# Performance work log

Measured on AMD Instinct MI355X. Metric: run time of the kernel, lower is better.

Reference implementation:

```python
import jax, jax.numpy as jnp
import numpy as np

INPUT_SIZE = 968
HIDDEN = 128
ESP = 1e-6


def _gru_scan(xp, w_hh, b_hh):
    # xp: [T, B, 3H] precomputed input projections; returns [T, B, H]
    B = xp.shape[1]
    h0 = jnp.zeros((B, HIDDEN), dtype=xp.dtype)

    def step(h, xp_t):
        gi_r, gi_z, gi_n = jnp.split(xp_t, 3, axis=-1)
        gh = h @ w_hh.T + b_hh
        gh_r, gh_z, gh_n = jnp.split(gh, 3, axis=-1)
        r = jax.nn.sigmoid(gi_r + gh_r)
        z = jax.nn.sigmoid(gi_z + gh_z)
        n = jnp.tanh(gi_n + r * gh_n)
        h_new = (1.0 - z) * n + z * h
        return h_new, h_new

    _, hs = jax.lax.scan(step, h0, xp)
    return hs


def _bigru_ln(x, w_ih_f, w_hh_f, b_ih_f, b_hh_f,
              w_ih_b, w_hh_b, b_ih_b, b_hh_b, ln_w, ln_b):
    # x: [B, T, D] (batch_first)
    # precompute input projections as one big GEMM per direction
    xp_f = jnp.einsum('btd,gd->btg', x, w_ih_f) + b_ih_f  # [B,T,3H]
    xp_b = jnp.einsum('btd,gd->btg', x, w_ih_b) + b_ih_b
    xp_f = jnp.swapaxes(xp_f, 0, 1)  # [T,B,3H]
    xp_b = jnp.swapaxes(xp_b, 0, 1)[::-1]  # reversed time for backward dir

    h_f = _gru_scan(xp_f, w_hh_f, b_hh_f)          # [T,B,H]
    h_b = _gru_scan(xp_b, w_hh_b, b_hh_b)[::-1]    # [T,B,H], un-reverse

    out = jnp.concatenate([h_f, h_b], axis=-1)     # [T,B,2H]
    out = jnp.swapaxes(out, 0, 1)                  # [B,T,2H]

    # LayerNormal: uses unbiased std (torch.std default, ddof=1), clamped
    mu = jnp.mean(out, axis=-1, keepdims=True)
    sigma = jnp.std(out, axis=-1, keepdims=True, ddof=1)
    sigma = jnp.maximum(sigma, ESP)
    return (out - mu) / sigma * ln_w + ln_b


def setup_inputs() -> dict:
    key = jax.random.key(0)
    ks = jax.random.split(key, 10)
    B, T = 64, 512
    s_ih = 1.0 / np.sqrt(HIDDEN)
    u = lambda k, shape: jax.random.uniform(k, shape, jnp.float32, -s_ih, s_ih)
    return {
        'x': jax.random.normal(ks[0], (B, T, INPUT_SIZE), jnp.float32),
        'w_ih_f': u(ks[1], (3 * HIDDEN, INPUT_SIZE)),
        'w_hh_f': u(ks[2], (3 * HIDDEN, HIDDEN)),
        'b_ih_f': u(ks[3], (3 * HIDDEN,)),
        'b_hh_f': u(ks[4], (3 * HIDDEN,)),
        'w_ih_b': u(ks[5], (3 * HIDDEN, INPUT_SIZE)),
        'w_hh_b': u(ks[6], (3 * HIDDEN, HIDDEN)),
        'b_ih_b': u(ks[7], (3 * HIDDEN,)),
        'b_hh_b': u(ks[8], (3 * HIDDEN,)),
        'ln_w': jnp.ones((2 * HIDDEN,), jnp.float32),
        'ln_b': jnp.zeros((2 * HIDDEN,), jnp.float32),
    }


def reference(x, w_ih_f, w_hh_f, b_ih_f, b_hh_f,
              w_ih_b, w_hh_b, b_ih_b, b_hh_b, ln_w, ln_b):
    return _bigru_ln(x, w_ih_f, w_hh_f, b_ih_f, b_hh_f,
                     w_ih_b, w_hh_b, b_ih_b, b_hh_b, ln_w, ln_b)
```

## Files before the change

kernel.cpp:

```cpp
#include <hip/hip_runtime.h>
#include <stdint.h>


#define LOG2E 1.4426950408889634f
#define TT 512
#define D_IN 968
#define KP 992
#define NOUT 768
#define HID 128

typedef __attribute__((ext_vector_type(8))) short short8;
typedef __attribute__((ext_vector_type(4))) float f32x4;
typedef __attribute__((ext_vector_type(4))) unsigned int u32x4;
typedef __attribute__((ext_vector_type(2))) unsigned int u32x2;

__device__ __forceinline__ unsigned short f2bf(float f) {
  unsigned u = __builtin_bit_cast(unsigned, f);
  u += 0x7FFFu + ((u >> 16) & 1u);
  return (unsigned short)(u >> 16);
}
__device__ __forceinline__ unsigned pack2bf(float a, float b) {
  return (unsigned)f2bf(a) | ((unsigned)f2bf(b) << 16);
}
__device__ __forceinline__ float exp2_(float x) { return __builtin_amdgcn_exp2f(x); }
__device__ __forceinline__ float rcp_(float x)  { return __builtin_amdgcn_rcpf(x); }

__device__ __forceinline__ void async_load16(const void* g, void* l) {
  __builtin_amdgcn_global_load_lds(
      (const __attribute__((address_space(1))) unsigned int*)g,
      (__attribute__((address_space(3))) unsigned int*)l, 16, 0, 0);
}

__device__ __forceinline__ void wg_barrier_lds() {
  asm volatile("s_waitcnt lgkmcnt(0)\n\ts_barrier" ::: "memory");
}

#define WIH_BYTES (NOUT * KP * 2)
#define WHH_BYTES (NOUT * HID * 2)
#define BIAS_BYTES 3072
#define BASE_OFF (WIH_BYTES + WHH_BYTES + BIAS_BYTES)
#define XBF_BYTES ((size_t)32768 * KP * 2)
#define XP_BYTES ((size_t)32768 * NOUT * 4)

__global__ __launch_bounds__(256) void kx_convert(const float* __restrict__ X,
                                                  unsigned short* __restrict__ Xb) {
  const long row = blockIdx.x;
  const int t = threadIdx.x;
  if (t < 242) {
    f32x4 v = *(const f32x4*)(X + row * D_IN + t * 4);
    u32x2 p = {pack2bf(v.x, v.y), pack2bf(v.z, v.w)};
    *(u32x2*)(Xb + row * KP + t * 4) = p;
  } else if (t < 248) {
    *(u32x2*)(Xb + row * KP + t * 4) = (u32x2){0, 0};
  }
}

__global__ __launch_bounds__(256) void k0_convert(
    const float* __restrict__ wihf, const float* __restrict__ whhf,
    const float* __restrict__ bihf, const float* __restrict__ wihb,
    const float* __restrict__ whhb, const float* __restrict__ bihb,
    unsigned short* __restrict__ wih16, unsigned short* __restrict__ whh16,
    float* __restrict__ bias_s) {
  int blk = blockIdx.x, tid = threadIdx.x;
  if (blk < NOUT) {
    int n = blk;
    float sc = ((n % 384) < 256) ? LOG2E : 2.0f * LOG2E;
    const float* src = (n < 384) ? (wihf + (long)n * D_IN) : (wihb + (long)(n - 384) * D_IN);
    for (int c = 0; c < 4; c++) {
      int k = c * 256 + tid;
      if (k < KP) {
        float v = (k < D_IN) ? src[k] * sc : 0.0f;
        wih16[(long)n * KP + k] = f2bf(v);
      }
    }
  } else if (blk < NOUT + 96) {
    int e0 = ((blk - NOUT) * 256 + tid) * 4;
    for (int i = 0; i < 4; i++) {
      int e = e0 + i;
      int m = e >> 7, k = e & 127;
      float sc = ((m % 384) < 256) ? LOG2E : 2.0f * LOG2E;
      float v = (m < 384) ? whhf[m * HID + k] : whhb[(m - 384) * HID + k];
      whh16[e] = f2bf(v * sc);
    }
  } else {
    for (int c = 0; c < 3; c++) {
      int n = c * 256 + tid;
      if (n < NOUT) {
        float sc = ((n % 384) < 256) ? LOG2E : 2.0f * LOG2E;
        bias_s[n] = ((n < 384) ? bihf[n] : bihb[n - 384]) * sc;
      }
    }
  }
}

__global__ __launch_bounds__(256, 2) void k1_gemm_fast(
    const unsigned short* __restrict__ Xb, const unsigned short* __restrict__ W,
    const float* __restrict__ bias_s, float* __restrict__ XP) {
  __shared__ unsigned short As[128 * 32];
  __shared__ unsigned short Bs[128 * 32];

  const int tid = threadIdx.x;
  const int lane = tid & 63, w = tid >> 6;
  const int q = lane >> 4, l15 = lane & 15;
  const int wr = w >> 1, wc = w & 1;
  const int nt = blockIdx.x;
  const int mt = blockIdx.y;
  const long R0 = (long)mt * 128;
  const int C0 = nt * 128;

  f32x4 acc[4][4];
#pragma unroll
  for (int i = 0; i < 4; i++)
#pragma unroll
    for (int j = 0; j < 4; j++) acc[i][j] = {0.f, 0.f, 0.f, 0.f};

  for (int it = 0; it < 31; it++) {
    const int k0 = it * 32;
#pragma unroll
    for (int c = 0; c < 2; c++) {
      int idx = c * 256 + w * 64 + lane;
      int row = idx >> 2, koff = (idx & 3) * 8;
      async_load16(Xb + (R0 + row) * KP + k0 + koff,
                   ((char*)As) + (c * 256 + w * 64) * 16);
      async_load16(W + (long)(C0 + row) * KP + k0 + koff,
                   ((char*)Bs) + (c * 256 + w * 64) * 16);
    }
    __syncthreads();
    short8 af[4], bf[4];
#pragma unroll
    for (int i = 0; i < 4; i++)
      af[i] = *(const short8*)&As[(wr * 64 + i * 16 + l15) * 32 + q * 8];
#pragma unroll
    for (int j = 0; j < 4; j++)
      bf[j] = *(const short8*)&Bs[(wc * 64 + j * 16 + l15) * 32 + q * 8];
#pragma unroll
    for (int i = 0; i < 4; i++)
#pragma unroll
      for (int j = 0; j < 4; j++)
        acc[i][j] = __builtin_amdgcn_mfma_f32_16x16x32_bf16(af[i], bf[j], acc[i][j], 0, 0, 0);
    __syncthreads();
  }
  float bv[4];
#pragma unroll
  for (int j = 0; j < 4; j++) bv[j] = bias_s[C0 + wc * 64 + j * 16 + l15];
#pragma unroll
  for (int i = 0; i < 4; i++)
#pragma unroll
    for (int j = 0; j < 4; j++) {
      int col = C0 + wc * 64 + j * 16 + l15;
      long Rb = R0 + wr * 64 + i * 16 + q * 4;
#pragma unroll
      for (int r = 0; r < 4; r++)
        XP[(Rb + r) * NOUT + col] = acc[i][j][r] + bv[j];
    }
}

#define AS_STRIDE 40
__global__ __launch_bounds__(256, 2) void k1_gemm_slow(
    const float* __restrict__ X, const unsigned short* __restrict__ W,
    const float* __restrict__ bias_s, float* __restrict__ XP) {
  __shared__ unsigned short As[128 * AS_STRIDE];
  __shared__ unsigned short Bs[128 * 32];
  const int tid = threadIdx.x;
  const int lane = tid & 63, w = tid >> 6;
  const int q = lane >> 4, l15 = lane & 15;
  const int wr = w >> 1, wc = w & 1;
  const int nt = blockIdx.x, mt = blockIdx.y;
  const long R0 = (long)mt * 128;
  const int C0 = nt * 128;
  const int ar = tid >> 1, ahf = tid & 1;
  f32x4 acc[4][4];
#pragma unroll
  for (int i = 0; i < 4; i++)
#pragma unroll
    for (int j = 0; j < 4; j++) acc[i][j] = {0.f, 0.f, 0.f, 0.f};
  const float* arow = X + (R0 + ar) * D_IN;
  for (int it = 0; it < 31; it++) {
    int k0 = it * 32;
    unsigned pk[8];
#pragma unroll
    for (int c = 0; c < 4; c++) {
      int kc = k0 + ahf * 16 + c * 4;
      kc = (kc <= 964) ? kc : 964;
      f32x4 v = *(const f32x4*)(arow + kc);
      pk[c * 2 + 0] = pack2bf(v.x, v.y);
      pk[c * 2 + 1] = pack2bf(v.z, v.w);
    }
    unsigned short* adst = &As[ar * AS_STRIDE + ahf * 16];
    *(u32x4*)adst = (u32x4){pk[0], pk[1], pk[2], pk[3]};
    *(u32x4*)(adst + 8) = (u32x4){pk[4], pk[5], pk[6], pk[7]};
#pragma unroll
    for (int c = 0; c < 2; c++) {
      int idx = c * 256 + w * 64 + lane;
      int brow = idx >> 2, koff = (idx & 3) * 8;
      async_load16(W + (long)(C0 + brow) * KP + k0 + koff,
                   ((char*)Bs) + (c * 256 + w * 64) * 16);
    }
    __syncthreads();
    short8 af[4], bf[4];
#pragma unroll
    for (int i = 0; i < 4; i++)
      af[i] = *(const short8*)&As[(wr * 64 + i * 16 + l15) * AS_STRIDE + q * 8];
#pragma unroll
    for (int j = 0; j < 4; j++)
      bf[j] = *(const short8*)&Bs[(wc * 64 + j * 16 + l15) * 32 + q * 8];
#pragma unroll
    for (int i = 0; i < 4; i++)
#pragma unroll
      for (int j = 0; j < 4; j++)
        acc[i][j] = __builtin_amdgcn_mfma_f32_16x16x32_bf16(af[i], bf[j], acc[i][j], 0, 0, 0);
    __syncthreads();
  }
  float bv[4];
#pragma unroll
  for (int j = 0; j < 4; j++) bv[j] = bias_s[C0 + wc * 64 + j * 16 + l15];
#pragma unroll
  for (int i = 0; i < 4; i++)
#pragma unroll
    for (int j = 0; j < 4; j++) {
      int col = C0 + wc * 64 + j * 16 + l15;
      long Rb = R0 + wr * 64 + i * 16 + q * 4;
#pragma unroll
      for (int r = 0; r < 4; r++)
        XP[(Rb + r) * NOUT + col] = acc[i][j][r] + bv[j];
    }
}

#define GI_STRIDE 52

__global__ __launch_bounds__(512) void k2_gru(
    const unsigned short* __restrict__ WHH, const float* __restrict__ XP,
    const float* __restrict__ bhh_f, const float* __restrict__ bhh_b,
    float* __restrict__ OUT) {
  __shared__ unsigned short Hl[2][16 * 128];
  __shared__ float GIl[2][8][16 * GI_STRIDE];

  const int tid = threadIdx.x;
  const int lane = tid & 63, w = tid >> 6;
  const int q = lane >> 4, b = lane & 15;
  const int dir = blockIdx.x & 1, bg = blockIdx.x >> 1;
  const int j0 = w * 16 + q * 4;

  for (int i = tid; i < 2 * 16 * 128; i += 512) ((unsigned short*)Hl)[i] = 0;

  short8 afr[3][4];
#pragma unroll
  for (int g = 0; g < 3; g++)
#pragma unroll
    for (int kt = 0; kt < 4; kt++) {
      int row = dir * 384 + g * 128 + w * 16 + b;
      afr[g][kt] = *(const short8*)(WHH + (long)row * HID + kt * 32 + q * 8);
    }
  const float* bhh = dir ? bhh_b : bhh_f;
  f32x4 bh[3];
#pragma unroll
  for (int g = 0; g < 3; g++) {
    f32x4 t = *(const f32x4*)(bhh + g * 128 + j0);
    bh[g] = t * ((g < 2) ? LOG2E : 2.0f * LOG2E);
  }

  const int lb = lane >> 2, lc = lane & 3;
  const long gi_base = (long)(bg * 16 + lb) * TT * NOUT + dir * 384 + w * 16 + lc * 4;
  const long out_base = (long)(bg * 16 + b) * TT * 256 + dir * 128 + j0;

  f32x4 gp0, gp1, gp2;
  {
    const int td0 = dir ? (TT - 1) : 0;
    const float* gb = XP + gi_base + (long)td0 * NOUT;
    f32x4 a0 = *(const f32x4*)(gb);
    f32x4 a1 = *(const f32x4*)(gb + 128);
    f32x4 a2 = *(const f32x4*)(gb + 256);
    float* giw0 = &GIl[0][w][lb * GI_STRIDE + lc * 4];
    *(f32x4*)(giw0 + 0) = a0;
    *(f32x4*)(giw0 + 16) = a1;
    *(f32x4*)(giw0 + 32) = a2;
    const int td1 = dir ? (TT - 2) : 1;
    const float* gb1 = XP + gi_base + (long)td1 * NOUT;
    gp0 = *(const f32x4*)(gb1);
    gp1 = *(const f32x4*)(gb1 + 128);
    gp2 = *(const f32x4*)(gb1 + 256);
  }
  f32x4 h = {0.f, 0.f, 0.f, 0.f};
  __syncthreads();

  for (int t = 0; t < TT; t++) {
    const int cur = t & 1, nxt = cur ^ 1;
    const int td = dir ? (TT - 1 - t) : t;

    short8 bfr[4];
#pragma unroll
    for (int kt = 0; kt < 4; kt++) {
      int ch = ((kt * 4 + q) ^ (b & 7)) * 8;
      bfr[kt] = *(const short8*)&Hl[cur][b * 128 + ch];
    }
    {
      float* giw = &GIl[nxt][w][lb * GI_STRIDE + lc * 4];
      *(f32x4*)(giw + 0) = gp0;
      *(f32x4*)(giw + 16) = gp1;
      *(f32x4*)(giw + 32) = gp2;
    }
    {
      int tn2 = (t + 2 < TT) ? t + 2 : TT - 1;
      int tdn2 = dir ? (TT - 1 - tn2) : tn2;
      const float* gb = XP + gi_base + (long)tdn2 * NOUT;
      gp0 = *(const f32x4*)(gb);
      gp1 = *(const f32x4*)(gb + 128);
      gp2 = *(const f32x4*)(gb + 256);
    }
    f32x4 accR = {0.f, 0.f, 0.f, 0.f};
    f32x4 accZ = {0.f, 0.f, 0.f, 0.f};
    f32x4 accN = {0.f, 0.f, 0.f, 0.f};
#pragma unroll
    for (int kt = 0; kt < 4; kt++) {
      accR = __builtin_amdgcn_mfma_f32_16x16x32_bf16(afr[0][kt], bfr[kt], accR, 0, 0, 0);
      accZ = __builtin_amdgcn_mfma_f32_16x16x32_bf16(afr[1][kt], bfr[kt], accZ, 0, 0, 0);
      accN = __builtin_amdgcn_mfma_f32_16x16x32_bf16(afr[2][kt], bfr[kt], accN, 0, 0, 0);
    }
    const float* gir = &GIl[cur][w][b * GI_STRIDE];
    f32x4 gr = *(const f32x4*)(gir + 0 + q * 4);
    f32x4 gz = *(const f32x4*)(gir + 16 + q * 4);
    f32x4 gn = *(const f32x4*)(gir + 32 + q * 4);
    f32x4 hnew;
#pragma unroll
    for (int i = 0; i < 4; i++) {
      float pr = gr[i] + accR[i] + bh[0][i];
      float pz = gz[i] + accZ[i] + bh[1][i];
      float r = rcp_(1.0f + exp2_(-pr));
      float z = rcp_(1.0f + exp2_(-pz));
      float pn = gn[i] + r * (accN[i] + bh[2][i]);
      float n = 1.0f - 2.0f * rcp_(exp2_(pn) + 1.0f);
      hnew[i] = n + z * (h[i] - n);
    }
    h = hnew;
    {
      int ch = ((j0 >> 3) ^ (b & 7)) * 8 + (j0 & 7);
      u32x2 hv = {pack2bf(hnew[0], hnew[1]), pack2bf(hnew[2], hnew[3])};
      *(u32x2*)&Hl[nxt][b * 128 + ch] = hv;
    }
    *(f32x4*)(OUT + out_base + (long)td * 256) = hnew;
    wg_barrier_lds();
  }
}

__global__ __launch_bounds__(256) void k3_ln(float* __restrict__ OUT,
                                             const float* __restrict__ lnw,
                                             const float* __restrict__ lnb) {
  const int tid = threadIdx.x, lane = tid & 63, w = tid >> 6;
  const long row = (long)blockIdx.x * 4 + w;
  float* p = OUT + row * 256 + lane * 4;
  f32x4 x = *(const f32x4*)p;
  float s = x[0] + x[1] + x[2] + x[3];
  float s2 = x[0] * x[0] + x[1] * x[1] + x[2] * x[2] + x[3] * x[3];
#pragma unroll
  for (int m = 1; m < 64; m <<= 1) {
    s += __shfl_xor(s, m, 64);
    s2 += __shfl_xor(s2, m, 64);
  }
  float mu = s * (1.0f / 256.0f);
  float var = (s2 - s * mu) * (1.0f / 255.0f);
  var = fmaxf(var, 0.0f);
  float sig = fmaxf(sqrtf(var), 1e-6f);
  float inv = 1.0f / sig;
  f32x4 wv = *(const f32x4*)(lnw + lane * 4);
  f32x4 bv = *(const f32x4*)(lnb + lane * 4);
  f32x4 y;
#pragma unroll
  for (int i = 0; i < 4; i++) y[i] = (x[i] - mu) * inv * wv[i] + bv[i];
  *(f32x4*)p = y;
}

extern "C" void kernel_launch(void* const* d_in, const int* in_sizes, int n_in,
                              void* d_out, int out_size, void* d_ws, size_t ws_size,
                              hipStream_t stream) {
  const float* x = (const float*)d_in[0];
  const float* wihf = (const float*)d_in[1];
  const float* whhf = (const float*)d_in[2];
  const float* bihf = (const float*)d_in[3];
  const float* bhhf = (const float*)d_in[4];
  const float* wihb = (const float*)d_in[5];
  const float* whhb = (const float*)d_in[6];
  const float* bihb = (const float*)d_in[7];
  const float* bhhb = (const float*)d_in[8];
  const float* lnw = (const float*)d_in[9];
  const float* lnb = (const float*)d_in[10];

  char* ws = (char*)d_ws;
  unsigned short* wih16 = (unsigned short*)ws;
  unsigned short* whh16 = (unsigned short*)(ws + WIH_BYTES);
  float* bias_s = (float*)(ws + WIH_BYTES + WHH_BYTES);
  float* out = (float*)d_out;

  const size_t need_fast = (size_t)BASE_OFF + XBF_BYTES + XP_BYTES;

  hipLaunchKernelGGL(k0_convert, dim3(768 + 96 + 1), dim3(256), 0, stream,
                     wihf, whhf, bihf, wihb, whhb, bihb, wih16, whh16, bias_s);

  float* xp;
  if (ws_size >= need_fast) {
    unsigned short* xbf = (unsigned short*)(ws + BASE_OFF);
    xp = (float*)(ws + BASE_OFF + XBF_BYTES);
    hipLaunchKernelGGL(kx_convert, dim3(32768), dim3(256), 0, stream, x, xbf);
    hipLaunchKernelGGL(k1_gemm_fast, dim3(6, 256), dim3(256), 0, stream,
                       xbf, wih16, bias_s, xp);
  } else {
    xp = (float*)(ws + BASE_OFF);
    hipLaunchKernelGGL(k1_gemm_slow, dim3(6, 256), dim3(256), 0, stream,
                       x, wih16, bias_s, xp);
  }
  hipLaunchKernelGGL(k2_gru, dim3(8), dim3(512), 0, stream, whh16, xp, bhhf, bhhb, out);
  hipLaunchKernelGGL(k3_ln, dim3(8192), dim3(256), 0, stream, out, lnw, lnb);
}
```

Before: 677.6 us.

## Prefetch GRU input projections into registers PF steps ahead, drop LDS staging

The GRU recurrence kernel no longer stages the precomputed input projections through a double-buffered LDS array. Each lane now loads its own gate inputs straight into a register ring that runs four timesteps ahead, and the time loop is unrolled by that depth. This removes the LDS writes and reads and the coalescing remap from the serial critical path. In exchange it uses more VGPRs and makes less coalesced global loads, which are 16-byte per-lane gathers across batch rows.

```diff
diff --git a/kernel.cpp b/kernel.cpp
--- a/kernel.cpp
+++ b/kernel.cpp
@@ -226,14 +226,13 @@
     }
 }
 
-#define GI_STRIDE 52
+#define PF 4
 
 __global__ __launch_bounds__(512) void k2_gru(
     const unsigned short* __restrict__ WHH, const float* __restrict__ XP,
     const float* __restrict__ bhh_f, const float* __restrict__ bhh_b,
     float* __restrict__ OUT) {
   __shared__ unsigned short Hl[2][16 * 128];
-  __shared__ float GIl[2][8][16 * GI_STRIDE];
 
   const int tid = threadIdx.x;
   const int lane = tid & 63, w = tid >> 6;
@@ -259,86 +258,72 @@
     bh[g] = t * ((g < 2) ? LOG2E : 2.0f * LOG2E);
   }
 
-  const int lb = lane >> 2, lc = lane & 3;
-  const long gi_base = (long)(bg * 16 + lb) * TT * NOUT + dir * 384 + w * 16 + lc * 4;
+  const long gi_base = (long)(bg * 16 + b) * TT * NOUT + dir * 384 + j0;
   const long out_base = (long)(bg * 16 + b) * TT * 256 + dir * 128 + j0;
 
-  f32x4 gp0, gp1, gp2;
-  {
-    const int td0 = dir ? (TT - 1) : 0;
-    const float* gb = XP + gi_base + (long)td0 * NOUT;
-    f32x4 a0 = *(const f32x4*)(gb);
-    f32x4 a1 = *(const f32x4*)(gb + 128);
-    f32x4 a2 = *(const f32x4*)(gb + 256);
-    float* giw0 = &GIl[0][w][lb * GI_STRIDE + lc * 4];
-    *(f32x4*)(giw0 + 0) = a0;
-    *(f32x4*)(giw0 + 16) = a1;
-    *(f32x4*)(giw0 + 32) = a2;
-    const int td1 = dir ? (TT - 2) : 1;
-    const float* gb1 = XP + gi_base + (long)td1 * NOUT;
-    gp0 = *(const f32x4*)(gb1);
-    gp1 = *(const f32x4*)(gb1 + 128);
-    gp2 = *(const f32x4*)(gb1 + 256);
+  f32x4 gR[PF], gZ[PF], gN[PF];
+#pragma unroll
+  for (int u = 0; u < PF; u++) {
+    const int td = dir ? (TT - 1 - u) : u;
+    const float* gb = XP + gi_base + (long)td * NOUT;
+    gR[u] = *(const f32x4*)(gb);
+    gZ[u] = *(const f32x4*)(gb + 128);
+    gN[u] = *(const f32x4*)(gb + 256);
   }
   f32x4 h = {0.f, 0.f, 0.f, 0.f};
   __syncthreads();
 
-  for (int t = 0; t < TT; t++) {
-    const int cur = t & 1, nxt = cur ^ 1;
-    const int td = dir ? (TT - 1 - t) : t;
-
-    short8 bfr[4];
-#pragma unroll
-    for (int kt = 0; kt < 4; kt++) {
-      int ch = ((kt * 4 + q) ^ (b & 7)) * 8;
-      bfr[kt] = *(const short8*)&Hl[cur][b * 128 + ch];
-    }
-    {
-      float* giw = &GIl[nxt][w][lb * GI_STRIDE + lc * 4];
-      *(f32x4*)(giw + 0) = gp0;
-      *(f32x4*)(giw + 16) = gp1;
-      *(f32x4*)(giw + 32) = gp2;
-    }
-    {
-      int tn2 = (t + 2 < TT) ? t + 2 : TT - 1;
-      int tdn2 = dir ? (TT - 1 - tn2) : tn2;
-      const float* gb = XP + gi_base + (long)tdn2 * NOUT;
-      gp0 = *(const f32x4*)(gb);
-      gp1 = *(const f32x4*)(gb + 128);
-      gp2 = *(const f32x4*)(gb + 256);
-    }
-    f32x4 accR = {0.f, 0.f, 0.f, 0.f};
-    f32x4 accZ = {0.f, 0.f, 0.f, 0.f};
-    f32x4 accN = {0.f, 0.f, 0.f, 0.f};
-#pragma unroll
-    for (int kt = 0; kt < 4; kt++) {
-      accR = __builtin_amdgcn_mfma_f32_16x16x32_bf16(afr[0][kt], bfr[kt], accR, 0, 0, 0);
-      accZ = __builtin_amdgcn_mfma_f32_16x16x32_bf16(afr[1][kt], bfr[kt], accZ, 0, 0, 0);
-      accN = __builtin_amdgcn_mfma_f32_16x16x32_bf16(afr[2][kt], bfr[kt], accN, 0, 0, 0);
-    }
-    const float* gir = &GIl[cur][w][b * GI_STRIDE];
-    f32x4 gr = *(const f32x4*)(gir + 0 + q * 4);
-    f32x4 gz = *(const f32x4*)(gir + 16 + q * 4);
-    f32x4 gn = *(const f32x4*)(gir + 32 + q * 4);
-    f32x4 hnew;
-#pragma unroll
-    for (int i = 0; i < 4; i++) {
-      float pr = gr[i] + accR[i] + bh[0][i];
-      float pz = gz[i] + accZ[i] + bh[1][i];
-      float r = rcp_(1.0f + exp2_(-pr));
-      float z = rcp_(1.0f + exp2_(-pz));
-      float pn = gn[i] + r * (accN[i] + bh[2][i]);
-      float n = 1.0f - 2.0f * rcp_(exp2_(pn) + 1.0f);
-      hnew[i] = n + z * (h[i] - n);
-    }
-    h = hnew;
-    {
-      int ch = ((j0 >> 3) ^ (b & 7)) * 8 + (j0 & 7);
-      u32x2 hv = {pack2bf(hnew[0], hnew[1]), pack2bf(hnew[2], hnew[3])};
-      *(u32x2*)&Hl[nxt][b * 128 + ch] = hv;
-    }
-    *(f32x4*)(OUT + out_base + (long)td * 256) = hnew;
-    wg_barrier_lds();
+  for (int t0 = 0; t0 < TT; t0 += PF) {
+#pragma unroll
+    for (int u = 0; u < PF; u++) {
+      const int t = t0 + u;
+      const int cur = t & 1, nxt = cur ^ 1;
+      const int td = dir ? (TT - 1 - t) : t;
+
+      short8 bfr[4];
+#pragma unroll
+      for (int kt = 0; kt < 4; kt++) {
+        int ch = ((kt * 4 + q) ^ (b & 7)) * 8;
+        bfr[kt] = *(const short8*)&Hl[cur][b * 128 + ch];
+      }
+      f32x4 accR = {0.f, 0.f, 0.f, 0.f};
+      f32x4 accZ = {0.f, 0.f, 0.f, 0.f};
+      f32x4 accN = {0.f, 0.f, 0.f, 0.f};
+#pragma unroll
+      for (int kt = 0; kt < 4; kt++) {
+        accR = __builtin_amdgcn_mfma_f32_16x16x32_bf16(afr[0][kt], bfr[kt], accR, 0, 0, 0);
+        accZ = __builtin_amdgcn_mfma_f32_16x16x32_bf16(afr[1][kt], bfr[kt], accZ, 0, 0, 0);
+        accN = __builtin_amdgcn_mfma_f32_16x16x32_bf16(afr[2][kt], bfr[kt], accN, 0, 0, 0);
+      }
+      f32x4 hnew;
+#pragma unroll
+      for (int i = 0; i < 4; i++) {
+        float pr = gR[u][i] + accR[i] + bh[0][i];
+        float pz = gZ[u][i] + accZ[i] + bh[1][i];
+        float r = rcp_(1.0f + exp2_(-pr));
+        float z = rcp_(1.0f + exp2_(-pz));
+        float pn = gN[u][i] + r * (accN[i] + bh[2][i]);
+        float n = 1.0f - 2.0f * rcp_(exp2_(pn) + 1.0f);
+        hnew[i] = n + z * (h[i] - n);
+      }
+      h = hnew;
+      {
+        int tn = t + PF;
+        tn = (tn < TT) ? tn : (TT - 1);
+        const int tdn = dir ? (TT - 1 - tn) : tn;
+        const float* gb = XP + gi_base + (long)tdn * NOUT;
+        gR[u] = *(const f32x4*)(gb);
+        gZ[u] = *(const f32x4*)(gb + 128);
+        gN[u] = *(const f32x4*)(gb + 256);
+      }
+      {
+        int ch = ((j0 >> 3) ^ (b & 7)) * 8 + (j0 & 7);
+        u32x2 hv = {pack2bf(hnew[0], hnew[1]), pack2bf(hnew[2], hnew[3])};
+        *(u32x2*)&Hl[nxt][b * 128 + ch] = hv;
+      }
+      *(f32x4*)(OUT + out_base + (long)td * 256) = hnew;
+      wg_barrier_lds();
+    }
   }
 }
 
```

Measured after the change: 683.2 us. No clear change (+0.8%).
